# Kernel tuning notes

Hardware: AMD Instinct MI355X
Metric: run time of the kernel (lower is better)

The kernel has to match this reference:

```python
import jax, jax.numpy as jnp
import numpy as np

EPS = 1e-8      # covariance regularizer (module-level `eps` in source repo)
ALPHA = 0.8     # style/content blend (module-level `alpha` in source repo)
SV_THRESH = 1e-5  # singular-value cutoff from the source


def _flatten(x):
    # x: [1, H, W, C] -> [C, H*W]
    xt = jnp.transpose(x[0], (2, 0, 1))  # C, H, W
    C = xt.shape[0]
    return xt.reshape(C, -1)


def _cov(f):
    # f: [C, N] already centered -> [C, C]
    C, N = f.shape
    return f @ f.T / (jnp.float32(N) - 1.0) + EPS * jnp.eye(C, dtype=f.dtype)


def _masked_pow(S, p):
    # Faithful to truncating columns with S <= 1e-5: zero their diag weight.
    mask = S > SV_THRESH
    S_safe = jnp.where(mask, S, 1.0)
    return jnp.where(mask, S_safe ** p, 0.0)


def setup_inputs() -> dict:
    key = jax.random.key(0)
    k1, k2 = jax.random.split(key)
    content = jax.random.normal(k1, (1, 128, 128, 512), dtype=jnp.float32)
    style = jax.random.normal(k2, (1, 128, 128, 512), dtype=jnp.float32)
    return {"content": content, "style": style}


def reference(content, style):
    H, W, C = content.shape[1], content.shape[2], content.shape[3]

    content_flat = _flatten(content)  # [C, Hc*Wc]
    style_flat = _flatten(style)      # [C, Hs*Ws]

    mc = content_flat.mean(axis=1, keepdims=True)
    fc = content_flat - mc
    ms = style_flat.mean(axis=1, keepdims=True)
    fs = style_flat - ms

    fcfc = _cov(fc)
    fsfs = _cov(fs)

    # tf.svd on a symmetric PSD matrix: S descending, U orthonormal.
    Uc, Sc, _ = jnp.linalg.svd(fcfc)
    Us, Ss, _ = jnp.linalg.svd(fsfs)

    # Whitening: Uc diag(Sc^-1/2) Uc^T (truncated cols == zeroed diag entries)
    Dc = _masked_pow(Sc, -0.5)
    whiten = (Uc * Dc[None, :]) @ Uc.T  # [C, C]
    fc_hat = whiten @ fc                # [C, N]

    # Coloring: Us diag(Ss^1/2) Us^T
    Ds = _masked_pow(Ss, 0.5)
    color = (Us * Ds[None, :]) @ Us.T
    fcs_hat = color @ fc_hat + ms

    blended = ALPHA * fcs_hat + (1.0 - ALPHA) * (fc + mc)  # [C, N]
    blended = blended.reshape(C, H, W)
    return jnp.transpose(blended, (1, 2, 0))[None]  # [1, H, W, C]
```

## Files before the change

kernel.cpp:

```cpp
#include <hip/hip_runtime.h>
#include <math.h>

#define NPIX 16384
#define CCH  512
#define MS   262144

typedef unsigned short u16;
typedef unsigned int u32;
typedef __attribute__((ext_vector_type(8))) short bf16x8;
typedef __attribute__((ext_vector_type(4))) float f32x4;

__device__ __forceinline__ u16 f2bf(float f) {
  u32 u = __builtin_bit_cast(u32, f);
  u += 0x7fffu + ((u >> 16) & 1u);
  return (u16)(u >> 16);
}
__device__ __forceinline__ float b2f(u16 h) {
  u32 u = ((u32)h) << 16;
  return __builtin_bit_cast(float, u);
}

typedef const __attribute__((address_space(1))) u32* gp_t;
typedef __attribute__((address_space(3))) u32* lp_t;
__device__ __forceinline__ void gl_lds16(const void* g, void* l) {
  __builtin_amdgcn_global_load_lds((gp_t)g, (lp_t)l, 16, 0, 0);
}

__device__ __forceinline__ void stage4(const u16* tile, size_t stride, int rl,
                                       int k0, u16* lds, int lane) {
  int lr = lane >> 4;
  int cg2 = (lane & 15) ^ ((rl + lr) & 15);
  gl_lds16(tile + (size_t)(rl + lr) * stride + k0 + cg2 * 8,
           lds + (size_t)rl * 128);
}
__device__ __forceinline__ bf16x8 fragld(const u16* lds, int row, int cl) {
  return *(const bf16x8*)&lds[(size_t)row * 128 + (size_t)((cl ^ (row & 15)) << 3)];
}

__device__ __forceinline__ void stage8_64(const u16* tile, size_t stride, int rl,
                                          int k0, u16* lds, int lane) {
  int lr = lane >> 3;
  int cg2 = (lane & 7) ^ ((rl + lr) & 7);
  gl_lds16(tile + (size_t)(rl + lr) * stride + k0 + cg2 * 8,
           lds + (size_t)rl * 64);
}
__device__ __forceinline__ bf16x8 fragld64(const u16* lds, int row, int cl) {
  return *(const bf16x8*)&lds[(size_t)row * 64 + (size_t)((cl ^ (row & 7)) << 3)];
}

__global__ __launch_bounds__(256) void prep_k(const float* __restrict__ Xc,
                                              const float* __restrict__ Xs,
                                              float* __restrict__ s16,
                                              u16* __restrict__ fct,
                                              u16* __restrict__ fcb) {
  int b = blockIdx.z;
  const float* X = b ? Xs : Xc;
  u16* outT = fct + (size_t)b * ((size_t)CCH * NPIX);
  __shared__ float T[64][65];
  __shared__ float red2[64][4];
  int n0 = blockIdx.x * 64, c0 = blockIdx.y * 64;
  int t = threadIdx.x;
  int cr = t & 15, nr = t >> 4;
  #pragma unroll
  for (int rr = 0; rr < 4; ++rr) {
    int n = nr + rr * 16;
    float4 v = *(const float4*)&X[(size_t)(n0 + n) * CCH + c0 + cr * 4];
    T[n][cr * 4 + 0] = v.x;
    T[n][cr * 4 + 1] = v.y;
    T[n][cr * 4 + 2] = v.z;
    T[n][cr * 4 + 3] = v.w;
    if (b == 0) {
      ushort4 q;
      q.x = f2bf(v.x); q.y = f2bf(v.y); q.z = f2bf(v.z); q.w = f2bf(v.w);
      *(ushort4*)&fcb[(size_t)(n0 + n) * CCH + c0 + cr * 4] = q;
    }
  }
  __syncthreads();
  int cl = t >> 2, np = (t & 3) * 16;
  size_t obase = (size_t)(c0 + cl) * NPIX + n0 + np;
  float s = 0.f;
  u16 ov[16];
  #pragma unroll
  for (int i = 0; i < 16; i += 4) {
    float v0 = T[np + i + 0][cl], v1 = T[np + i + 1][cl];
    float v2 = T[np + i + 2][cl], v3 = T[np + i + 3][cl];
    s += v0 + v1 + v2 + v3;
    ov[i + 0] = f2bf(v0); ov[i + 1] = f2bf(v1);
    ov[i + 2] = f2bf(v2); ov[i + 3] = f2bf(v3);
  }
  *(bf16x8*)&outT[obase + 0] = *(bf16x8*)&ov[0];
  *(bf16x8*)&outT[obase + 8] = *(bf16x8*)&ov[8];
  red2[cl][t & 3] = s;
  __syncthreads();
  if (t < 64) {
    float cs = red2[t][0] + red2[t][1] + red2[t][2] + red2[t][3];
    atomicAdd(&s16[(blockIdx.x & 15) * 1024 + b * CCH + c0 + t], cs);
  }
}

__global__ __launch_bounds__(256, 2) void gram_part(const u16* __restrict__ fct,
                                                    float* __restrict__ Gp,
                                                    const float* __restrict__ s16,
                                                    float* __restrict__ sums) {
  int kc = blockIdx.x;
  int pair = blockIdx.y;
  int b = blockIdx.z;
  int tid = threadIdx.x;
  if (kc == 0 && pair == 0) {
    #pragma unroll
    for (int c = tid; c < CCH; c += 256) {
      float s = 0.f;
      #pragma unroll
      for (int k = 0; k < 16; ++k) s += s16[k * 1024 + b * CCH + c];
      sums[b * CCH + c] = s;
    }
  }
  int bi = pair >> 2, bj = pair & 3;
  const u16* Xb = fct + (size_t)b * ((size_t)CCH * NPIX);
  __shared__ u16 As[2][128 * 64];
  __shared__ u16 Bs[2][128 * 64];
  int w = tid >> 6, lane = tid & 63;
  int qm = w & 1, qn = w >> 1;
  const u16* ssrc = (w < 2) ? Xb + (size_t)(bi * 128) * NPIX
                            : Xb + (size_t)(bj * 128) * NPIX;
  int rbase = (w & 1) * 64;
  f32x4 acc[4][4];
  #pragma unroll
  for (int t = 0; t < 4; ++t)
    #pragma unroll
    for (int u = 0; u < 4; ++u) acc[t][u] = (f32x4)(0.f);

  #pragma unroll
  for (int i = 0; i < 8; ++i)
    stage8_64(ssrc, NPIX, rbase + i * 8, kc * 1024, (w < 2) ? As[0] : Bs[0], lane);
  __syncthreads();

  for (int st = 0; st < 16; ++st) {
    int cur = st & 1;
    if (st < 15) {
      int k0n = kc * 1024 + (st + 1) * 64;
      #pragma unroll
      for (int i = 0; i < 8; ++i)
        stage8_64(ssrc, NPIX, rbase + i * 8, k0n,
                  (w < 2) ? As[cur ^ 1] : Bs[cur ^ 1], lane);
    }
    #pragma unroll
    for (int s = 0; s < 2; ++s) {
      int cl = s * 4 + (lane >> 4);
      bf16x8 a[4], bb[4];
      #pragma unroll
      for (int t = 0; t < 4; ++t) a[t] = fragld64(As[cur], qm * 64 + t * 16 + (lane & 15), cl);
      #pragma unroll
      for (int u = 0; u < 4; ++u) bb[u] = fragld64(Bs[cur], qn * 64 + u * 16 + (lane & 15), cl);
      #pragma unroll
      for (int t = 0; t < 4; ++t)
        #pragma unroll
        for (int u = 0; u < 4; ++u)
          acc[t][u] = __builtin_amdgcn_mfma_f32_16x16x32_bf16(a[t], bb[u], acc[t][u], 0, 0, 0);
    }
    __syncthreads();
  }
  size_t tbase = ((size_t)(b * 16 + kc) * 16 + pair) * 16384;
  #pragma unroll
  for (int t = 0; t < 4; ++t) {
    int row0 = qm * 64 + t * 16 + (lane >> 4) * 4;
    #pragma unroll
    for (int u = 0; u < 4; ++u) {
      int col = qn * 64 + u * 16 + (lane & 15);
      #pragma unroll
      for (int r4 = 0; r4 < 4; ++r4)
        Gp[tbase + (size_t)(row0 + r4) * 128 + col] = acc[t][u][r4];
    }
  }
}

__global__ __launch_bounds__(256) void gram_reduce(const float* __restrict__ Gp,
                                                   const float* __restrict__ sums,
                                                   float* __restrict__ cov,
                                                   float* __restrict__ rowsum) {
  int idx = blockIdx.x * 256 + threadIdx.x;
  int b = idx >> 18;
  int ij = idx & (MS - 1);
  int i = ij >> 9, j = ij & 511;
  int pair = ((i >> 7) << 2) | (j >> 7);
  int lij = ((i & 127) << 7) | (j & 127);
  size_t base = ((size_t)(b * 16) * 16 + pair) * 16384 + lij;
  float g = 0.f;
  #pragma unroll
  for (int kc = 0; kc < 16; ++kc)
    g += Gp[base + (size_t)kc * (16 * 16384)];
  const float* s = sums + b * CCH;
  float v = (g - s[i] * s[j] * (1.f / (float)NPIX)) * (1.f / (float)(NPIX - 1));
  if (i == j) v += 1e-8f;
  cov[idx] = v;
  __shared__ float red[256];
  int t = threadIdx.x;
  red[t] = fabsf(v);
  __syncthreads();
  for (int st = 128; st > 0; st >>= 1) {
    if (t < st) red[t] += red[t + st];
    __syncthreads();
  }
  if (t == 0) atomicAdd(&rowsum[b * CCH + i], red[0]);
}

__global__ __launch_bounds__(256) void nsinit_k(const float* __restrict__ cov,
                                                const float* __restrict__ rowsum,
                                                float* __restrict__ snorm,
                                                float* __restrict__ coef,
                                                u16* __restrict__ Anh,
                                                u16* __restrict__ Anl,
                                                u16* __restrict__ Z0) {
  __shared__ float red[256];
  int tid = threadIdx.x, blk = blockIdx.x;
  float m = fmaxf(rowsum[tid], rowsum[tid + 256]);
  red[tid] = m; __syncthreads();
  for (int s = 128; s > 0; s >>= 1) {
    if (tid < s) red[tid] = fmaxf(red[tid], red[tid + s]);
    __syncthreads();
  }
  float snc = red[0]; __syncthreads();
  m = fmaxf(rowsum[512 + tid], rowsum[768 + tid]);
  red[tid] = m; __syncthreads();
  for (int s = 128; s > 0; s >>= 1) {
    if (tid < s) red[tid] = fmaxf(red[tid], red[tid + s]);
    __syncthreads();
  }
  float sns = red[0];
  if (blk == 0 && tid == 0) {
    snorm[0] = snc; snorm[1] = sns;
    coef[0] = 0.8f * sqrtf(sns / snc);
  }
  int idx = blk * 256 + tid;
  int b = idx >> 18;
  int ij = idx & (MS - 1);
  int diag = (ij >> 9) == (ij & 511);
  float av = cov[idx] * (b ? 1.f / sns : 1.f / snc);
  u16 hi = f2bf(av);
  Anh[idx] = hi;
  Anl[idx] = f2bf(av - b2f(hi));
  float t0 = (diag ? 3.f - av : -av) * 0.70710678f;
  Z0[idx] = f2bf(t0);
}

struct MM16 {
  const u16* A[4];
  const u16* B[4];
  void* D[4];
  float scale, diag;
  int outFp32;
};

__global__ __launch_bounds__(256) void mm16_k(MM16 args) {
  int z = blockIdx.z;
  const u16* __restrict__ A = args.A[z];
  const u16* __restrict__ B = args.B[z];
  int bi = blockIdx.y, bj = blockIdx.x;
  __shared__ u16 As[2][32 * 128];
  __shared__ u16 Bs[2][64 * 128];
  int tid = threadIdx.x, w = tid >> 6, lane = tid & 63;
  int qm = w & 1, qn = w >> 1;
  const u16* ssrc = (w < 2) ? A + (size_t)(bi * 32) * CCH
                            : B + (size_t)(bj * 64) * CCH;
  int rbase = (w < 2) ? (w & 1) * 16 : (w & 1) * 32;
  f32x4 acc[2];
  acc[0] = (f32x4)(0.f); acc[1] = (f32x4)(0.f);

  if (w < 2) {
    #pragma unroll
    for (int i = 0; i < 4; ++i) stage4(ssrc, CCH, rbase + i * 4, 0, As[0], lane);
  } else {
    #pragma unroll
    for (int i = 0; i < 8; ++i) stage4(ssrc, CCH, rbase + i * 4, 0, Bs[0], lane);
  }
  __syncthreads();

  for (int st = 0; st < 4; ++st) {
    int cur = st & 1;
    if (st < 3) {
      int k0 = (st + 1) * 128;
      if (w < 2) {
        #pragma unroll
        for (int i = 0; i < 4; ++i) stage4(ssrc, CCH, rbase + i * 4, k0, As[cur ^ 1], lane);
      } else {
        #pragma unroll
        for (int i = 0; i < 8; ++i) stage4(ssrc, CCH, rbase + i * 4, k0, Bs[cur ^ 1], lane);
      }
    }
    #pragma unroll
    for (int s = 0; s < 4; ++s) {
      int cl = s * 4 + (lane >> 4);
      bf16x8 a = fragld(As[cur], qm * 16 + (lane & 15), cl);
      bf16x8 b0 = fragld(Bs[cur], qn * 32 + (lane & 15), cl);
      bf16x8 b1 = fragld(Bs[cur], qn * 32 + 16 + (lane & 15), cl);
      acc[0] = __builtin_amdgcn_mfma_f32_16x16x32_bf16(a, b0, acc[0], 0, 0, 0);
      acc[1] = __builtin_amdgcn_mfma_f32_16x16x32_bf16(a, b1, acc[1], 0, 0, 0);
    }
    __syncthreads();
  }
  float sc = args.scale;
  int row0 = bi * 32 + qm * 16 + (lane >> 4) * 4;
  #pragma unroll
  for (int u = 0; u < 2; ++u) {
    int col = bj * 64 + qn * 32 + u * 16 + (lane & 15);
    #pragma unroll
    for (int r4 = 0; r4 < 4; ++r4) {
      float v = sc * acc[u][r4];
      if (row0 + r4 == col) v += args.diag;
      size_t o = (size_t)(row0 + r4) * CCH + col;
      if (args.outFp32) ((float*)args.D[z])[o] = v;
      else ((u16*)args.D[z])[o] = f2bf(v);
    }
  }
}

__global__ __launch_bounds__(256) void symsplit_k(const float* __restrict__ src,
                                                  u16* __restrict__ hi,
                                                  u16* __restrict__ lo) {
  int b = blockIdx.y;
  int ij = blockIdx.x * 256 + threadIdx.x;
  int i = ij >> 9, j = ij & 511;
  size_t base = (size_t)b * MS;
  float v = 0.5f * (src[base + ij] + src[base + (size_t)j * CCH + i]);
  u16 h = f2bf(v);
  hi[base + ij] = h;
  lo[base + ij] = f2bf(v - b2f(h));
}

struct MMS {
  const u16 *Ah[4], *Al[4], *Bh[4], *Bl[4];
  const u16 *Eh[4], *El[4];
  u16 *Dh[4], *Dl[4];
  float *D32[4];
  u16 *Db[4];
  float scale, beta;
  const float* coefPtr;
};

__global__ __launch_bounds__(256) void mmsplit_k(MMS args) {
  int z = blockIdx.z;
  int bi = blockIdx.y, bj = blockIdx.x;
  __shared__ u16 Ash[2][32 * 64], Asl[2][32 * 64];
  __shared__ u16 Bsh[2][64 * 64], Bsl[2][64 * 64];
  int tid = threadIdx.x, w = tid >> 6, lane = tid & 63;
  int qm = w & 1, qn = w >> 1;
  const u16* sp = (w == 0) ? args.Ah[z] : (w == 1) ? args.Al[z]
                : (w == 2) ? args.Bh[z] : args.Bl[z];
  const u16* ssrc = sp + (size_t)(((w < 2) ? bi * 32 : bj * 64)) * CCH;
  u16* sd0 = (w == 0) ? Ash[0] : (w == 1) ? Asl[0] : (w == 2) ? Bsh[0] : Bsl[0];
  u16* sd1 = (w == 0) ? Ash[1] : (w == 1) ? Asl[1] : (w == 2) ? Bsh[1] : Bsl[1];
  int nst = (w < 2) ? 4 : 8;
  f32x4 acc[2];
  acc[0] = (f32x4)(0.f); acc[1] = (f32x4)(0.f);

  for (int i = 0; i < nst; ++i)
    stage8_64(ssrc, CCH, i * 8, 0, sd0, lane);
  __syncthreads();

  for (int st = 0; st < 8; ++st) {
    int cur = st & 1;
    if (st < 7) {
      u16* sdn = cur ? sd0 : sd1;
      for (int i = 0; i < nst; ++i)
        stage8_64(ssrc, CCH, i * 8, (st + 1) * 64, sdn, lane);
    }
    #pragma unroll
    for (int s = 0; s < 2; ++s) {
      int cl = s * 4 + (lane >> 4);
      int arow = qm * 16 + (lane & 15);
      bf16x8 ah = fragld64(Ash[cur], arow, cl);
      bf16x8 al = fragld64(Asl[cur], arow, cl);
      bf16x8 bh[2], bl[2];
      #pragma unroll
      for (int u = 0; u < 2; ++u) {
        int brow = qn * 32 + u * 16 + (lane & 15);
        bh[u] = fragld64(Bsh[cur], brow, cl);
        bl[u] = fragld64(Bsl[cur], brow, cl);
      }
      #pragma unroll
      for (int u = 0; u < 2; ++u) {
        acc[u] = __builtin_amdgcn_mfma_f32_16x16x32_bf16(ah, bh[u], acc[u], 0, 0, 0);
        acc[u] = __builtin_amdgcn_mfma_f32_16x16x32_bf16(ah, bl[u], acc[u], 0, 0, 0);
        acc[u] = __builtin_amdgcn_mfma_f32_16x16x32_bf16(al, bh[u], acc[u], 0, 0, 0);
      }
    }
    __syncthreads();
  }
  float sc = args.scale;
  if (args.coefPtr) sc *= *args.coefPtr;
  int row0 = bi * 32 + qm * 16 + (lane >> 4) * 4;
  #pragma unroll
  for (int u = 0; u < 2; ++u) {
    int col = bj * 64 + qn * 32 + u * 16 + (lane & 15);
    #pragma unroll
    for (int r4 = 0; r4 < 4; ++r4) {
      size_t o = (size_t)(row0 + r4) * CCH + col;
      float v = sc * acc[u][r4];
      if (args.beta != 0.f) v += args.beta * (b2f(args.Eh[z][o]) + b2f(args.El[z][o]));
      if (args.D32[z]) args.D32[z][o] = v;
      if (args.Dh[z]) {
        u16 h = f2bf(v);
        args.Dh[z][o] = h;
        args.Dl[z][o] = f2bf(v - b2f(h));
      }
      if (args.Db[z]) args.Db[z][o] = f2bf(v);
    }
  }
}

__global__ __launch_bounds__(256) void mconst_k(const u16* __restrict__ Mb,
                                                const float* __restrict__ sums,
                                                float* __restrict__ mconst) {
  int c = blockIdx.x * 8 + (threadIdx.x >> 5);
  int l = threadIdx.x & 31;
  float s = 0.f;
  #pragma unroll
  for (int k = 0; k < 16; ++k) {
    int j = l + 32 * k;
    s += b2f(Mb[(size_t)c * CCH + j]) * sums[j];
  }
  s += __shfl_down(s, 16, 32);
  s += __shfl_down(s, 8, 32);
  s += __shfl_down(s, 4, 32);
  s += __shfl_down(s, 2, 32);
  s += __shfl_down(s, 1, 32);
  if (l == 0) mconst[c] = (0.8f * sums[512 + c] - s) * (1.f / (float)NPIX);
}

__global__ __launch_bounds__(256) void apply_mfma(const u16* __restrict__ fcb,
                                                  const u16* __restrict__ Mb,
                                                  const float* __restrict__ mconst,
                                                  const float* __restrict__ X,
                                                  float* __restrict__ out) {
  int bi = blockIdx.y;
  int bj = blockIdx.x;
  __shared__ u16 As[2][128 * 64];
  __shared__ u16 Bs[2][128 * 64];
  int tid = threadIdx.x, w = tid >> 6, lane = tid & 63;
  int qm = w & 1, qn = w >> 1;
  const u16* ssrc = (w < 2) ? fcb + (size_t)(bi * 128) * CCH
                            : Mb + (size_t)(bj * 128) * CCH;
  int rbase = (w & 1) * 64;
  f32x4 acc[4][4];
  #pragma unroll
  for (int t = 0; t < 4; ++t)
    #pragma unroll
    for (int u = 0; u < 4; ++u) acc[t][u] = (f32x4)(0.f);

  #pragma unroll
  for (int i = 0; i < 8; ++i)
    stage8_64(ssrc, CCH, rbase + i * 8, 0, (w < 2) ? As[0] : Bs[0], lane);
  __syncthreads();

  for (int st = 0; st < 8; ++st) {
    int cur = st & 1;
    if (st < 7) {
      #pragma unroll
      for (int i = 0; i < 8; ++i)
        stage8_64(ssrc, CCH, rbase + i * 8, (st + 1) * 64,
                  (w < 2) ? As[cur ^ 1] : Bs[cur ^ 1], lane);
    }
    #pragma unroll
    for (int s = 0; s < 2; ++s) {
      int cl = s * 4 + (lane >> 4);
      bf16x8 a[4], bb[4];
      #pragma unroll
      for (int t = 0; t < 4; ++t) a[t] = fragld64(As[cur], qm * 64 + t * 16 + (lane & 15), cl);
      #pragma unroll
      for (int u = 0; u < 4; ++u) bb[u] = fragld64(Bs[cur], qn * 64 + u * 16 + (lane & 15), cl);
      #pragma unroll
      for (int t = 0; t < 4; ++t)
        #pragma unroll
        for (int u = 0; u < 4; ++u)
          acc[t][u] = __builtin_amdgcn_mfma_f32_16x16x32_bf16(a[t], bb[u], acc[t][u], 0, 0, 0);
    }
    __syncthreads();
  }
  #pragma unroll
  for (int t = 0; t < 4; ++t) {
    int row0 = bi * 128 + qm * 64 + t * 16 + (lane >> 4) * 4;
    #pragma unroll
    for (int u = 0; u < 4; ++u) {
      int col = bj * 128 + qn * 64 + u * 16 + (lane & 15);
      float cst = mconst[col];
      #pragma unroll
      for (int r4 = 0; r4 < 4; ++r4) {
        size_t o = (size_t)(row0 + r4) * CCH + col;
        out[o] = acc[t][u][r4] + cst + 0.2f * X[o];
      }
    }
  }
}

extern "C" void kernel_launch(void* const* d_in, const int* in_sizes, int n_in,
                              void* d_out, int out_size, void* d_ws, size_t ws_size,
                              hipStream_t stream) {
  const float* Xc = (const float*)d_in[0];
  const float* Xs = (const float*)d_in[1];
  float* out = (float*)d_out;

  float* f = (float*)d_ws;
  float* sums   = f;
  float* rowsum = f + 1024;
  float* s16    = f + 2048;
  float* cov    = f + 2048 + 2 * MS;
  float* snorm  = cov + 2 * MS;
  float* coef   = snorm + 8;
  float* mconst = coef + 8;
  float* Zf     = mconst + 512;

  float* Gp = (float*)d_out;

  u16* h   = (u16*)(Zf + 2 * MS);
  u16* fct = h;
  u16* fcb = h + (size_t)2 * CCH * NPIX;
  const size_t B2 = 2 * MS;
  u16* Anh  = fct + 0 * B2;
  u16* Anl  = fct + 1 * B2;
  u16* Y1   = fct + 2 * B2;
  u16* Ya   = fct + 3 * B2;
  u16* Z0   = fct + 4 * B2;
  u16* Z1   = fct + 5 * B2;
  u16* Tb   = fct + 6 * B2;
  u16* Zfsh = fct + 7 * B2;
  u16* Zfsl = fct + 8 * B2;
  u16* Ph   = fct + 9 * B2;
  u16* Pl   = fct + 10 * B2;
  u16* Qh   = fct + 11 * B2;
  u16* Ql   = fct + 12 * B2;
  u16* Zrsh = fct + 13 * B2;
  u16* Zrsl = fct + 14 * B2;
  u16* W2h  = fct + 15 * B2;
  u16* W2l  = W2h + MS;
  u16* Mb   = W2l + MS;

  hipMemsetAsync(d_ws, 0, (2048 + 16384) * sizeof(float), stream);

  prep_k<<<dim3(256, 8, 2), 256, 0, stream>>>(Xc, Xs, s16, fct, fcb);
  gram_part<<<dim3(16, 16, 2), 256, 0, stream>>>(fct, Gp, s16, sums);
  gram_reduce<<<2048, 256, 0, stream>>>(Gp, sums, cov, rowsum);
  nsinit_k<<<2048, 256, 0, stream>>>(cov, rowsum, snorm, coef, Anh, Anl, Z0);

  {
    MM16 y1{};
    y1.A[0] = Anh;      y1.B[0] = Z0;      y1.D[0] = Y1;
    y1.A[1] = Anh + MS; y1.B[1] = Z0 + MS; y1.D[1] = Y1 + MS;
    y1.scale = 1.f; y1.diag = 0.f; y1.outFp32 = 0;
    mm16_k<<<dim3(8, 16, 2), 256, 0, stream>>>(y1);
  }
  {
    MM16 t{};
    t.A[0] = Z0;      t.B[0] = Y1;      t.D[0] = Tb;
    t.A[1] = Z0 + MS; t.B[1] = Y1 + MS; t.D[1] = Tb + MS;
    t.scale = -1.f; t.diag = 3.f; t.outFp32 = 0;
    mm16_k<<<dim3(8, 16, 2), 256, 0, stream>>>(t);
  }
  {
    MM16 yz{};
    yz.A[0] = Y1;      yz.B[0] = Tb;      yz.D[0] = Ya;
    yz.A[1] = Y1 + MS; yz.B[1] = Tb + MS; yz.D[1] = Ya + MS;
    yz.A[2] = Tb;      yz.B[2] = Z0;      yz.D[2] = Z1;
    yz.A[3] = Tb + MS; yz.B[3] = Z0 + MS; yz.D[3] = Z1 + MS;
    yz.scale = 0.5f; yz.diag = 0.f; yz.outFp32 = 0;
    mm16_k<<<dim3(8, 16, 4), 256, 0, stream>>>(yz);
  }
  {
    MM16 t{};
    t.A[0] = Z1;      t.B[0] = Ya;      t.D[0] = Tb;
    t.A[1] = Z1 + MS; t.B[1] = Ya + MS; t.D[1] = Tb + MS;
    t.scale = -1.f; t.diag = 3.f; t.outFp32 = 0;
    mm16_k<<<dim3(8, 16, 2), 256, 0, stream>>>(t);
  }
  {
    MM16 yz{};
    yz.A[0] = Ya;      yz.B[0] = Tb;      yz.D[0] = Y1;
    yz.A[1] = Ya + MS; yz.B[1] = Tb + MS; yz.D[1] = Y1 + MS;
    yz.A[2] = Tb;      yz.B[2] = Z1;      yz.D[2] = Z0;
    yz.A[3] = Tb + MS; yz.B[3] = Z1 + MS; yz.D[3] = Z0 + MS;
    yz.scale = 0.5f; yz.diag = 0.f; yz.outFp32 = 0;
    mm16_k<<<dim3(8, 16, 4), 256, 0, stream>>>(yz);
  }
  {
    MM16 t{};
    t.A[0] = Z0;      t.B[0] = Y1;      t.D[0] = Tb;
    t.A[1] = Z0 + MS; t.B[1] = Y1 + MS; t.D[1] = Tb + MS;
    t.scale = -1.f; t.diag = 3.f; t.outFp32 = 0;
    mm16_k<<<dim3(8, 16, 2), 256, 0, stream>>>(t);
  }
  {
    MM16 zf{};
    zf.A[0] = Tb;      zf.B[0] = Z0;      zf.D[0] = Zf;
    zf.A[1] = Tb + MS; zf.B[1] = Z0 + MS; zf.D[1] = Zf + MS;
    zf.scale = 0.5f; zf.diag = 0.f; zf.outFp32 = 1;
    mm16_k<<<dim3(8, 16, 2), 256, 0, stream>>>(zf);
  }

  symsplit_k<<<dim3(1024, 2), 256, 0, stream>>>(Zf, Zfsh, Zfsl);

  MMS pq{};
  for (int b = 0; b < 2; ++b) {
    pq.Ah[b] = Zfsh + b * MS; pq.Al[b] = Zfsl + b * MS;
    pq.Bh[b] = Anh + b * MS;  pq.Bl[b] = Anl + b * MS;
    pq.Dh[b] = Ph + b * MS;   pq.Dl[b] = Pl + b * MS;
    pq.Ah[2 + b] = Zfsh + b * MS; pq.Al[2 + b] = Zfsl + b * MS;
    pq.Bh[2 + b] = Zfsh + b * MS; pq.Bl[2 + b] = Zfsl + b * MS;
    pq.Dh[2 + b] = Qh + b * MS;   pq.Dl[2 + b] = Ql + b * MS;
  }
  pq.scale = 1.f;
  mmsplit_k<<<dim3(8, 16, 4), 256, 0, stream>>>(pq);

  MMS zr{};
  for (int b = 0; b < 2; ++b) {
    zr.Ah[b] = Ph + b * MS;   zr.Al[b] = Pl + b * MS;
    zr.Bh[b] = Qh + b * MS;   zr.Bl[b] = Ql + b * MS;
    zr.Eh[b] = Zfsh + b * MS; zr.El[b] = Zfsl + b * MS;
    zr.D32[b] = Zf + b * MS;
  }
  zr.scale = -0.5f; zr.beta = 1.5f;
  mmsplit_k<<<dim3(8, 16, 2), 256, 0, stream>>>(zr);

  symsplit_k<<<dim3(1024, 2), 256, 0, stream>>>(Zf, Zrsh, Zrsl);

  MMS wv{};
  wv.Ah[0] = Anh + MS;  wv.Al[0] = Anl + MS;
  wv.Bh[0] = Zrsh + MS; wv.Bl[0] = Zrsl + MS;
  wv.Dh[0] = W2h; wv.Dl[0] = W2l;
  wv.scale = 1.f;
  mmsplit_k<<<dim3(8, 16, 1), 256, 0, stream>>>(wv);

  MMS mv{};
  mv.Ah[0] = W2h;  mv.Al[0] = W2l;
  mv.Bh[0] = Zrsh; mv.Bl[0] = Zrsl;
  mv.Db[0] = Mb;
  mv.scale = 1.f; mv.coefPtr = coef;
  mmsplit_k<<<dim3(8, 16, 1), 256, 0, stream>>>(mv);

  mconst_k<<<64, 256, 0, stream>>>(Mb, sums, mconst);
  apply_mfma<<<dim3(4, 128), 256, 0, stream>>>(fcb, Mb, mconst, Xc, out);
}
```

Baseline: 268.0 us.

## Retile Gram partial kernel to 64x128 tiles with 32-wide K steps

The Gram partial-sum kernel moves from 128x128 output tiles with a 64-wide K stage to 64x128 tiles with a 32-wide K stage. This doubles the grid, shrinks LDS and accumulator use per block, and raises launch bounds to four blocks per CU. The goal is more blocks resident on the 256 CUs and better latency hiding. In exchange, each K step does fewer MFMAs per barrier, the A rows are reloaded across more tiles, and gram_reduce's indexing is updated to the new partial layout.

```diff
diff --git a/kernel.cpp b/kernel.cpp
--- a/kernel.cpp
+++ b/kernel.cpp
@@ -46,6 +46,17 @@
 }
 __device__ __forceinline__ bf16x8 fragld64(const u16* lds, int row, int cl) {
   return *(const bf16x8*)&lds[(size_t)row * 64 + (size_t)((cl ^ (row & 7)) << 3)];
+}
+
+__device__ __forceinline__ void stage16_32(const u16* tile, size_t stride, int rl,
+                                           int k0, u16* lds, int lane) {
+  int lr = lane >> 2;
+  int cg2 = (lane & 3) ^ ((rl + lr) & 3);
+  gl_lds16(tile + (size_t)(rl + lr) * stride + k0 + cg2 * 8,
+           lds + (size_t)rl * 32);
+}
+__device__ __forceinline__ bf16x8 fragld32(const u16* lds, int row, int cl) {
+  return *(const bf16x8*)&lds[(size_t)row * 32 + (size_t)((cl ^ (row & 3)) << 3)];
 }
 
 __global__ __launch_bounds__(256) void prep_k(const float* __restrict__ Xc,
@@ -98,15 +109,16 @@
   }
 }
 
-__global__ __launch_bounds__(256, 2) void gram_part(const u16* __restrict__ fct,
+__global__ __launch_bounds__(256, 4) void gram_part(const u16* __restrict__ fct,
                                                     float* __restrict__ Gp,
                                                     const float* __restrict__ s16,
                                                     float* __restrict__ sums) {
   int kc = blockIdx.x;
-  int pair = blockIdx.y;
+  int rp = blockIdx.y >> 2;
+  int cp = blockIdx.y & 3;
   int b = blockIdx.z;
   int tid = threadIdx.x;
-  if (kc == 0 && pair == 0) {
+  if (kc == 0 && blockIdx.y == 0) {
     #pragma unroll
     for (int c = tid; c < CCH; c += 256) {
       float s = 0.f;
@@ -115,58 +127,62 @@
       sums[b * CCH + c] = s;
     }
   }
-  int bi = pair >> 2, bj = pair & 3;
   const u16* Xb = fct + (size_t)b * ((size_t)CCH * NPIX);
-  __shared__ u16 As[2][128 * 64];
-  __shared__ u16 Bs[2][128 * 64];
+  __shared__ u16 As[2][64 * 32];
+  __shared__ u16 Bs[2][128 * 32];
   int w = tid >> 6, lane = tid & 63;
-  int qm = w & 1, qn = w >> 1;
-  const u16* ssrc = (w < 2) ? Xb + (size_t)(bi * 128) * NPIX
-                            : Xb + (size_t)(bj * 128) * NPIX;
-  int rbase = (w & 1) * 64;
-  f32x4 acc[4][4];
+  const u16* srcA = Xb + (size_t)(rp * 64) * NPIX;
+  const u16* srcB = Xb + (size_t)(cp * 128) * NPIX;
+  f32x4 acc[4][2];
   #pragma unroll
   for (int t = 0; t < 4; ++t)
     #pragma unroll
-    for (int u = 0; u < 4; ++u) acc[t][u] = (f32x4)(0.f);
-
-  #pragma unroll
-  for (int i = 0; i < 8; ++i)
-    stage8_64(ssrc, NPIX, rbase + i * 8, kc * 1024, (w < 2) ? As[0] : Bs[0], lane);
+    for (int u = 0; u < 2; ++u) acc[t][u] = (f32x4)(0.f);
+
+  #define STAGE_G(buf, k0)                                                   \
+    if (w == 0)      { stage16_32(srcA, NPIX, 0, k0, As[buf], lane);         \
+                       stage16_32(srcA, NPIX, 16, k0, As[buf], lane); }      \
+    else if (w == 1) { stage16_32(srcA, NPIX, 32, k0, As[buf], lane);        \
+                       stage16_32(srcA, NPIX, 48, k0, As[buf], lane); }      \
+    else if (w == 2) { stage16_32(srcB, NPIX, 0, k0, Bs[buf], lane);         \
+                       stage16_32(srcB, NPIX, 16, k0, Bs[buf], lane);        \
+                       stage16_32(srcB, NPIX, 32, k0, Bs[buf], lane);        \
+                       stage16_32(srcB, NPIX, 48, k0, Bs[buf], lane); }      \
+    else             { stage16_32(srcB, NPIX, 64, k0, Bs[buf], lane);        \
+                       stage16_32(srcB, NPIX, 80, k0, Bs[buf], lane);        \
+                       stage16_32(srcB, NPIX, 96, k0, Bs[buf], lane);        \
+                       stage16_32(srcB, NPIX, 112, k0, Bs[buf], lane); }
+
+  STAGE_G(0, kc * 1024);
   __syncthreads();
 
-  for (int st = 0; st < 16; ++st) {
+  for (int st = 0; st < 32; ++st) {
     int cur = st & 1;
-    if (st < 15) {
-      int k0n = kc * 1024 + (st + 1) * 64;
-      #pragma unroll
-      for (int i = 0; i < 8; ++i)
-        stage8_64(ssrc, NPIX, rbase + i * 8, k0n,
-                  (w < 2) ? As[cur ^ 1] : Bs[cur ^ 1], lane);
-    }
-    #pragma unroll
-    for (int s = 0; s < 2; ++s) {
-      int cl = s * 4 + (lane >> 4);
-      bf16x8 a[4], bb[4];
-      #pragma unroll
-      for (int t = 0; t < 4; ++t) a[t] = fragld64(As[cur], qm * 64 + t * 16 + (lane & 15), cl);
-      #pragma unroll
-      for (int u = 0; u < 4; ++u) bb[u] = fragld64(Bs[cur], qn * 64 + u * 16 + (lane & 15), cl);
-      #pragma unroll
-      for (int t = 0; t < 4; ++t)
-        #pragma unroll
-        for (int u = 0; u < 4; ++u)
-          acc[t][u] = __builtin_amdgcn_mfma_f32_16x16x32_bf16(a[t], bb[u], acc[t][u], 0, 0, 0);
-    }
+    if (st < 31) {
+      int k0n = kc * 1024 + (st + 1) * 32;
+      STAGE_G(cur ^ 1, k0n);
+    }
+    int cl = lane >> 4;
+    bf16x8 a[4], bb[2];
+    #pragma unroll
+    for (int t = 0; t < 4; ++t) a[t] = fragld32(As[cur], t * 16 + (lane & 15), cl);
+    #pragma unroll
+    for (int u = 0; u < 2; ++u) bb[u] = fragld32(Bs[cur], w * 32 + u * 16 + (lane & 15), cl);
+    #pragma unroll
+    for (int t = 0; t < 4; ++t)
+      #pragma unroll
+      for (int u = 0; u < 2; ++u)
+        acc[t][u] = __builtin_amdgcn_mfma_f32_16x16x32_bf16(a[t], bb[u], acc[t][u], 0, 0, 0);
     __syncthreads();
   }
-  size_t tbase = ((size_t)(b * 16 + kc) * 16 + pair) * 16384;
+  #undef STAGE_G
+  size_t tbase = ((size_t)(b * 16 + kc) * 32 + rp * 4 + cp) * 8192;
   #pragma unroll
   for (int t = 0; t < 4; ++t) {
-    int row0 = qm * 64 + t * 16 + (lane >> 4) * 4;
-    #pragma unroll
-    for (int u = 0; u < 4; ++u) {
-      int col = qn * 64 + u * 16 + (lane & 15);
+    int row0 = t * 16 + (lane >> 4) * 4;
+    #pragma unroll
+    for (int u = 0; u < 2; ++u) {
+      int col = w * 32 + u * 16 + (lane & 15);
       #pragma unroll
       for (int r4 = 0; r4 < 4; ++r4)
         Gp[tbase + (size_t)(row0 + r4) * 128 + col] = acc[t][u][r4];
@@ -182,13 +198,13 @@
   int b = idx >> 18;
   int ij = idx & (MS - 1);
   int i = ij >> 9, j = ij & 511;
-  int pair = ((i >> 7) << 2) | (j >> 7);
-  int lij = ((i & 127) << 7) | (j & 127);
-  size_t base = ((size_t)(b * 16) * 16 + pair) * 16384 + lij;
+  int tile = (i >> 6) * 4 + (j >> 7);
+  int lij = ((i & 63) << 7) | (j & 127);
+  size_t base = ((size_t)(b * 16) * 32 + tile) * 8192 + lij;
   float g = 0.f;
   #pragma unroll
   for (int kc = 0; kc < 16; ++kc)
-    g += Gp[base + (size_t)kc * (16 * 16384)];
+    g += Gp[base + (size_t)kc * (32 * 8192)];
   const float* s = sums + b * CCH;
   float v = (g - s[i] * s[j] * (1.f / (float)NPIX)) * (1.f / (float)(NPIX - 1));
   if (i == j) v += 1e-8f;
@@ -537,7 +553,7 @@
   hipMemsetAsync(d_ws, 0, (2048 + 16384) * sizeof(float), stream);
 
   prep_k<<<dim3(256, 8, 2), 256, 0, stream>>>(Xc, Xs, s16, fct, fcb);
-  gram_part<<<dim3(16, 16, 2), 256, 0, stream>>>(fct, Gp, s16, sums);
+  gram_part<<<dim3(16, 32, 2), 256, 0, stream>>>(fct, Gp, s16, sums);
   gram_reduce<<<2048, 256, 0, stream>>>(Gp, sums, cov, rowsum);
   nsinit_k<<<2048, 256, 0, stream>>>(cov, rowsum, snorm, coef, Anh, Anl, Z0);
 
```

Measured after the change: 272.9 us. Within noise of the previous version (+1.8%).
